# Performance work log

Hardware: AMD Instinct MI355X
Metric: run time of the kernel (lower is better)

## Reference

```python
import jax, jax.numpy as jnp
import numpy as np

N_NODES = 100000
N_EDGES = 1600000
NUM_FEATURES = 128
HIDDEN_DIM = 64
NUM_CLASSES = 2
NUM_GRAPHS = 128


def setup_inputs() -> dict:
    key = jax.random.key(0)
    ks = jax.random.split(key, 9)
    x = jax.random.normal(ks[0], (N_NODES, NUM_FEATURES), dtype=jnp.float32)
    edge_index = jax.random.randint(ks[1], (2, N_EDGES), 0, N_NODES, dtype=jnp.int64)
    batch = jnp.sort(jax.random.randint(ks[2], (N_NODES,), 0, NUM_GRAPHS, dtype=jnp.int64))
    # GCNConv weights (PyG: glorot-init linear, zero bias; values here arbitrary for a numeric baseline)
    s1 = 1.0 / np.sqrt(NUM_FEATURES)
    s2 = 1.0 / np.sqrt(HIDDEN_DIM)
    W1 = jax.random.uniform(ks[3], (NUM_FEATURES, HIDDEN_DIM), jnp.float32, -s1, s1)
    b1 = jax.random.uniform(ks[4], (HIDDEN_DIM,), jnp.float32, -s1, s1)
    W2 = jax.random.uniform(ks[5], (HIDDEN_DIM, HIDDEN_DIM), jnp.float32, -s2, s2)
    b2 = jax.random.uniform(ks[6], (HIDDEN_DIM,), jnp.float32, -s2, s2)
    Wf = jax.random.uniform(ks[7], (HIDDEN_DIM, NUM_CLASSES), jnp.float32, -s2, s2)
    bf = jax.random.uniform(ks[8], (NUM_CLASSES,), jnp.float32, -s2, s2)
    return {"x": x, "edge_index": edge_index, "batch": batch,
            "W1": W1, "b1": b1, "W2": W2, "b2": b2, "Wf": Wf, "bf": bf}


def _gcn_aggregate(h, src, dst, norm, n_nodes):
    # messages: gather source features, scale by sym-norm coefficient, scatter-add at targets
    msg = h[src] * norm[:, None]                       # [E+N, F]
    return jax.ops.segment_sum(msg, dst, num_segments=n_nodes)


def reference(x, edge_index, batch, W1, b1, W2, b2, Wf, bf):
    n = x.shape[0]
    loops = jnp.arange(n, dtype=edge_index.dtype)
    # GCNConv adds self-loops and uses symmetric normalization D^{-1/2}(A+I)D^{-1/2}
    src = jnp.concatenate([edge_index[0], loops])
    dst = jnp.concatenate([edge_index[1], loops])
    deg = jax.ops.segment_sum(jnp.ones_like(dst, dtype=x.dtype), dst, num_segments=n)
    dis = jnp.where(deg > 0, jax.lax.rsqrt(jnp.maximum(deg, 1.0)), 0.0)
    norm = dis[src] * dis[dst]                         # per-edge coefficient

    h = jax.nn.relu(_gcn_aggregate(x @ W1, src, dst, norm, n) + b1)
    h = jax.nn.relu(_gcn_aggregate(h @ W2, src, dst, norm, n) + b2)

    # global_mean_pool over batch segment ids
    sums = jax.ops.segment_sum(h, batch, num_segments=NUM_GRAPHS)
    counts = jax.ops.segment_sum(jnp.ones((n,), dtype=h.dtype), batch, num_segments=NUM_GRAPHS)
    pooled = sums / jnp.maximum(counts, 1.0)[:, None]  # [G, hidden]

    return pooled @ Wf + bf                            # [G, num_classes]
```

## Files before the change

kernel.cpp:

```cpp
#include <hip/hip_runtime.h>
#include <hip/hip_bf16.h>


constexpr int F_IN   = 128;
constexpr int HID    = 64;
constexpr int NGRAPH = 128;
constexpr int NCLS   = 2;

constexpr int EPB = 4096;
constexpr int NB  = 391;
constexpr int DPB = 256;
constexpr int ST  = 56;
constexpr int NOCT = ST / 8;

typedef __attribute__((ext_vector_type(8))) short bf16x8;
typedef __attribute__((ext_vector_type(4))) float f32x4;

__device__ __forceinline__ float bf2f(unsigned short s) {
    union { unsigned u; float f; } v; v.u = ((unsigned)s) << 16; return v.f;
}
__device__ __forceinline__ unsigned short f2bf(float f) {
    union { float f; unsigned u; } v; v.f = f;
    unsigned u = v.u;
    return (unsigned short)((u + 0x7FFFu + ((u >> 16) & 1u)) >> 16);
}
__device__ __forceinline__ void unpack8(uint4 g, float* f) {
    union { unsigned u; float x; } v;
    v.u = g.x << 16; f[0] = v.x;  v.u = g.x & 0xFFFF0000u; f[1] = v.x;
    v.u = g.y << 16; f[2] = v.x;  v.u = g.y & 0xFFFF0000u; f[3] = v.x;
    v.u = g.z << 16; f[4] = v.x;  v.u = g.z & 0xFFFF0000u; f[5] = v.x;
    v.u = g.w << 16; f[6] = v.x;  v.u = g.w & 0xFFFF0000u; f[7] = v.x;
}

__global__ __launch_bounds__(256) void k_bin2(const int* __restrict__ srcv,
                                              const int* __restrict__ dstv,
                                              int* __restrict__ gcur,
                                              unsigned* __restrict__ bin,
                                              int E, int cap) {
    __shared__ int h[NB];
    __shared__ int base[NB];
    for (int i = threadIdx.x; i < NB; i += 256) h[i] = 0;
    __syncthreads();
    int e0 = blockIdx.x * EPB, e1 = min(e0 + EPB, E);
    for (int e = e0 + threadIdx.x; e < e1; e += 256)
        atomicAdd(&h[dstv[e] >> 8], 1);
    __syncthreads();
    for (int i = threadIdx.x; i < NB; i += 256) {
        int c = h[i];
        base[i] = (c > 0) ? atomicAdd(&gcur[i], c) : 0;
        h[i] = 0;
    }
    __syncthreads();
    for (int e = e0 + threadIdx.x; e < e1; e += 256) {
        int d = dstv[e], s = srcv[e];
        int b = d >> 8;
        int pos = base[b] + atomicAdd(&h[b], 1);
        bin[(size_t)b * cap + pos] = ((unsigned)(d & 255) << 20) | (unsigned)s;
    }
}

__global__ __launch_bounds__(256) void k_ell(const unsigned* __restrict__ bin,
                                             const int* __restrict__ bktCnt,
                                             int* __restrict__ ellg,
                                             int* __restrict__ cntg,
                                             float* __restrict__ disg,
                                             int N, int cap) {
    __shared__ int lcnt[DPB];
    __shared__ int lell[DPB * ST];
    int b = blockIdx.x;
    for (int i = threadIdx.x; i < DPB; i += 256) lcnt[i] = 0;
    for (int i = threadIdx.x; i < DPB * ST; i += 256) lell[i] = -1;
    __syncthreads();
    int n = bktCnt[b];
    const unsigned* src = bin + (size_t)b * cap;
    for (int i = threadIdx.x; i < n; i += 256) {
        unsigned p = src[i];
        int d = (int)(p >> 20);
        int s = (int)(p & 0xFFFFF);
        int pos = atomicAdd(&lcnt[d], 1);
        if (pos < ST) lell[d * ST + pos] = s;
    }
    __syncthreads();
    int base = b * DPB;
    int lim = (N - base) * ST;
    if (lim > DPB * ST) lim = DPB * ST;
    int* dst = ellg + (size_t)base * ST;
    for (int i = threadIdx.x; i < lim; i += 256) dst[i] = lell[i];
    for (int i = threadIdx.x; i < DPB; i += 256) {
        int r = base + i;
        if (r < N) {
            int c = min(lcnt[i], ST);
            cntg[r] = c;
            disg[r] = rsqrtf((float)c + 1.0f);
        }
    }
}

__global__ __launch_bounds__(256) void k_gemm_f(const float* __restrict__ X,
                                                const float* __restrict__ W,
                                                unsigned short* __restrict__ Y,
                                                int M) {
    constexpr int SRX = 136;
    constexpr int SRW = 136;
    __shared__ unsigned short Xs[128 * SRX];
    __shared__ unsigned short Wt[64 * SRW];
    const int t = threadIdx.x;
    const int row0 = blockIdx.x * 128;

#pragma unroll
    for (int i = 0; i < 16; ++i) {
        int idx = i * 256 + t;
        int r = idx >> 5, c4 = idx & 31;
        int gr = row0 + r;
        float4 v = (gr < M) ? *(const float4*)&X[(size_t)gr * 128 + c4 * 4]
                            : float4{0.f, 0.f, 0.f, 0.f};
        uint2 p{f2bf(v.x) | ((unsigned)f2bf(v.y) << 16),
                f2bf(v.z) | ((unsigned)f2bf(v.w) << 16)};
        *(uint2*)&Xs[r * SRX + c4 * 4] = p;
    }
#pragma unroll
    for (int i = 0; i < 8; ++i) {
        int idx = i * 256 + t;
        int k = idx >> 4, n4 = idx & 15;
        float4 v = *(const float4*)&W[(size_t)k * 64 + n4 * 4];
        Wt[(n4 * 4 + 0) * SRW + k] = f2bf(v.x);
        Wt[(n4 * 4 + 1) * SRW + k] = f2bf(v.y);
        Wt[(n4 * 4 + 2) * SRW + k] = f2bf(v.z);
        Wt[(n4 * 4 + 3) * SRW + k] = f2bf(v.w);
    }
    __syncthreads();

    const int ln = t & 63, wv = t >> 6;
    const int m16 = ln & 15, kg = ln >> 4;
    const int rbase = wv * 32;
    f32x4 acc[2][4];
#pragma unroll
    for (int i = 0; i < 2; ++i)
#pragma unroll
        for (int j = 0; j < 4; ++j) acc[i][j] = f32x4{0.f, 0.f, 0.f, 0.f};

#pragma unroll
    for (int ks = 0; ks < 4; ++ks) {
        bf16x8 a0 = *(const bf16x8*)&Xs[(rbase + m16) * SRX + ks * 32 + kg * 8];
        bf16x8 a1 = *(const bf16x8*)&Xs[(rbase + 16 + m16) * SRX + ks * 32 + kg * 8];
#pragma unroll
        for (int ct = 0; ct < 4; ++ct) {
            bf16x8 b = *(const bf16x8*)&Wt[(ct * 16 + m16) * SRW + ks * 32 + kg * 8];
            acc[0][ct] = __builtin_amdgcn_mfma_f32_16x16x32_bf16(a0, b, acc[0][ct], 0, 0, 0);
            acc[1][ct] = __builtin_amdgcn_mfma_f32_16x16x32_bf16(a1, b, acc[1][ct], 0, 0, 0);
        }
    }

    __syncthreads();
    unsigned short* Cs = Xs;
#pragma unroll
    for (int mt = 0; mt < 2; ++mt)
#pragma unroll
        for (int ct = 0; ct < 4; ++ct)
#pragma unroll
            for (int reg = 0; reg < 4; ++reg) {
                int r = rbase + mt * 16 + kg * 4 + reg;
                Cs[r * 64 + ct * 16 + m16] = f2bf(acc[mt][ct][reg]);
            }
    __syncthreads();
#pragma unroll
    for (int i = 0; i < 4; ++i) {
        int idx = i * 256 + t;
        int r = idx >> 3, c8 = idx & 7;
        int gr = row0 + r;
        if (gr < M)
            *(uint4*)&Y[(size_t)gr * 64 + c8 * 8] = *(const uint4*)&Cs[r * 64 + c8 * 8];
    }
}

__global__ __launch_bounds__(256) void k_gemm_b(const unsigned short* __restrict__ X,
                                                const float* __restrict__ W,
                                                unsigned short* __restrict__ Y,
                                                int M) {
    constexpr int SRX = 72;
    constexpr int SRW = 72;
    __shared__ unsigned short Xs[128 * SRX];
    __shared__ unsigned short Wt[64 * SRW];
    const int t = threadIdx.x;
    const int row0 = blockIdx.x * 128;

#pragma unroll
    for (int i = 0; i < 4; ++i) {
        int idx = i * 256 + t;
        int r = idx >> 3, c8 = idx & 7;
        int gr = row0 + r;
        uint4 v = (gr < M) ? *(const uint4*)&X[(size_t)gr * 64 + c8 * 8]
                           : uint4{0u, 0u, 0u, 0u};
        *(uint4*)&Xs[r * SRX + c8 * 8] = v;
    }
#pragma unroll
    for (int i = 0; i < 4; ++i) {
        int idx = i * 256 + t;
        int k = idx >> 4, n4 = idx & 15;
        float4 v = *(const float4*)&W[(size_t)k * 64 + n4 * 4];
        Wt[(n4 * 4 + 0) * SRW + k] = f2bf(v.x);
        Wt[(n4 * 4 + 1) * SRW + k] = f2bf(v.y);
        Wt[(n4 * 4 + 2) * SRW + k] = f2bf(v.z);
        Wt[(n4 * 4 + 3) * SRW + k] = f2bf(v.w);
    }
    __syncthreads();

    const int ln = t & 63, wv = t >> 6;
    const int m16 = ln & 15, kg = ln >> 4;
    const int rbase = wv * 32;
    f32x4 acc[2][4];
#pragma unroll
    for (int i = 0; i < 2; ++i)
#pragma unroll
        for (int j = 0; j < 4; ++j) acc[i][j] = f32x4{0.f, 0.f, 0.f, 0.f};

#pragma unroll
    for (int ks = 0; ks < 2; ++ks) {
        bf16x8 a0 = *(const bf16x8*)&Xs[(rbase + m16) * SRX + ks * 32 + kg * 8];
        bf16x8 a1 = *(const bf16x8*)&Xs[(rbase + 16 + m16) * SRX + ks * 32 + kg * 8];
#pragma unroll
        for (int ct = 0; ct < 4; ++ct) {
            bf16x8 b = *(const bf16x8*)&Wt[(ct * 16 + m16) * SRW + ks * 32 + kg * 8];
            acc[0][ct] = __builtin_amdgcn_mfma_f32_16x16x32_bf16(a0, b, acc[0][ct], 0, 0, 0);
            acc[1][ct] = __builtin_amdgcn_mfma_f32_16x16x32_bf16(a1, b, acc[1][ct], 0, 0, 0);
        }
    }

    __syncthreads();
    unsigned short* Cs = Xs;
#pragma unroll
    for (int mt = 0; mt < 2; ++mt)
#pragma unroll
        for (int ct = 0; ct < 4; ++ct)
#pragma unroll
            for (int reg = 0; reg < 4; ++reg) {
                int r = rbase + mt * 16 + kg * 4 + reg;
                Cs[r * 64 + ct * 16 + m16] = f2bf(acc[mt][ct][reg]);
            }
    __syncthreads();
#pragma unroll
    for (int i = 0; i < 4; ++i) {
        int idx = i * 256 + t;
        int r = idx >> 3, c8 = idx & 7;
        int gr = row0 + r;
        if (gr < M)
            *(uint4*)&Y[(size_t)gr * 64 + c8 * 8] = *(const uint4*)&Cs[r * 64 + c8 * 8];
    }
}

__global__ __launch_bounds__(256) void k_gather(const unsigned short* __restrict__ h,
                                                const int* __restrict__ ell,
                                                const int* __restrict__ cnt,
                                                const float* __restrict__ dis,
                                                const float* __restrict__ b,
                                                unsigned short* __restrict__ outb,
                                                int N) {
    int wave = (blockIdx.x * 256 + threadIdx.x) >> 6;
    int lane = threadIdx.x & 63;
    int nq   = lane >> 3;
    int sl   = lane & 7;
    int node = wave * 8 + nq;
    bool valid = node < N;
    int nc = valid ? node : N - 1;

    int deg  = cnt[nc];
    float dd = dis[nc];
    const uint4* h4 = (const uint4*)h;

    int raws[NOCT];
#pragma unroll
    for (int o = 0; o < NOCT; ++o)
        raws[o] = (o * 8 + sl < deg) ? ell[(size_t)nc * ST + o * 8 + sl] : -1;

    int   idxs[NOCT];
    float wsv[NOCT];
#pragma unroll
    for (int o = 0; o < NOCT; ++o) {
        idxs[o] = (raws[o] >= 0) ? raws[o] : 0;
        wsv[o]  = (raws[o] >= 0) ? dis[idxs[o]] * dd : 0.f;
    }

    float acc[8], tmp[8];
    unpack8(h4[(size_t)nc * 8 + sl], acc);
    float sw = dd * dd;
    float4 bv0 = *(const float4*)&b[sl * 8];
    float4 bv1 = *(const float4*)&b[sl * 8 + 4];
    acc[0] = acc[0] * sw + bv0.x; acc[1] = acc[1] * sw + bv0.y;
    acc[2] = acc[2] * sw + bv0.z; acc[3] = acc[3] * sw + bv0.w;
    acc[4] = acc[4] * sw + bv1.x; acc[5] = acc[5] * sw + bv1.y;
    acc[6] = acc[6] * sw + bv1.z; acc[7] = acc[7] * sw + bv1.w;

#pragma unroll
    for (int o = 0; o < NOCT; ++o) {
        if (o * 8 < deg) {
#pragma unroll
            for (int jj = 0; jj < 8; ++jj) {
                int   s  = __shfl(idxs[o], nq * 8 + jj, 64);
                float wj = __shfl(wsv[o],  nq * 8 + jj, 64);
                uint4 g = h4[(size_t)s * 8 + sl];
                unpack8(g, tmp);
#pragma unroll
                for (int q = 0; q < 8; ++q)
                    acc[q] = fmaf(tmp[q], wj, acc[q]);
            }
        }
    }
    if (valid) {
        uint4 p;
        p.x = f2bf(fmaxf(acc[0], 0.f)) | ((unsigned)f2bf(fmaxf(acc[1], 0.f)) << 16);
        p.y = f2bf(fmaxf(acc[2], 0.f)) | ((unsigned)f2bf(fmaxf(acc[3], 0.f)) << 16);
        p.z = f2bf(fmaxf(acc[4], 0.f)) | ((unsigned)f2bf(fmaxf(acc[5], 0.f)) << 16);
        p.w = f2bf(fmaxf(acc[6], 0.f)) | ((unsigned)f2bf(fmaxf(acc[7], 0.f)) << 16);
        ((uint4*)outb)[(size_t)node * 8 + sl] = p;
    }
}

constexpr int POOL_CHUNK = 16;
__global__ __launch_bounds__(256) void k_pool(const unsigned short* __restrict__ h,
                                              const int* __restrict__ batch,
                                              float* __restrict__ sums,
                                              float* __restrict__ gcnt, int N) {
    int wave = (blockIdx.x * 256 + threadIdx.x) >> 6;
    int lane = threadIdx.x & 63;
    int n0 = wave * POOL_CHUNK;
    if (n0 >= N) return;
    int n1 = min(n0 + POOL_CHUNK, N);

    int   gcur = batch[n0];
    float acc  = 0.f;
    int   run  = 0;
    for (int n = n0; n < n1; ++n) {
        int g = batch[n];
        if (g != gcur) {
            atomicAdd(&sums[gcur * HID + lane], acc);
            if (lane == 0) atomicAdd(&gcnt[gcur], (float)run);
            gcur = g; acc = 0.f; run = 0;
        }
        acc += bf2f(h[(size_t)n * HID + lane]);
        ++run;
    }
    atomicAdd(&sums[gcur * HID + lane], acc);
    if (lane == 0) atomicAdd(&gcnt[gcur], (float)run);
}

__global__ __launch_bounds__(256) void k_final(const float* __restrict__ sums,
                                               const float* __restrict__ gcnt,
                                               const float* __restrict__ Wf,
                                               const float* __restrict__ bfv,
                                               float* __restrict__ out) {
    int t = threadIdx.x;
    int g = t >> 1, c = t & 1;
    float invc = 1.0f / fmaxf(gcnt[g], 1.0f);
    float acc = bfv[c];
#pragma unroll
    for (int k = 0; k < HID; ++k)
        acc = fmaf(sums[g * HID + k] * invc, Wf[k * NCLS + c], acc);
    out[g * NCLS + c] = acc;
}

extern "C" void kernel_launch(void* const* d_in, const int* in_sizes, int n_in,
                              void* d_out, int out_size, void* d_ws, size_t ws_size,
                              hipStream_t stream) {
    const float* x   = (const float*)d_in[0];
    const int*   ei  = (const int*)d_in[1];
    const int*   bat = (const int*)d_in[2];
    const float* W1  = (const float*)d_in[3];
    const float* b1  = (const float*)d_in[4];
    const float* W2  = (const float*)d_in[5];
    const float* b2  = (const float*)d_in[6];
    const float* Wf  = (const float*)d_in[7];
    const float* bfv = (const float*)d_in[8];
    float* out = (float*)d_out;

    const int N = in_sizes[0] / F_IN;
    const int E = in_sizes[1] / 2;
    const int* srcv = ei;
    const int* dstv = ei + E;

    const int nblk = (E + EPB - 1) / EPB;
    const int cap  = E / NB + 1280;

    const size_t S2 = (size_t)N * HID * 2;
    char* ws = (char*)d_ws;
    unsigned short* bufA = (unsigned short*)ws;
    unsigned short* bufB = (unsigned short*)(ws + S2);
    int*   ell  = (int*)(ws + 2 * S2);
    char*  tail = ws + 2 * S2 + (size_t)N * ST * 4;
    int*   cnt  = (int*)tail;
    float* dis  = (float*)(tail + (size_t)N * 4);
    float* sums = (float*)(tail + (size_t)N * 8);
    float* gcnt = sums + NGRAPH * HID;
    int*   gcur = (int*)(gcnt + NGRAPH);

    unsigned* bin = (unsigned*)bufA;

    hipMemsetAsync(sums, 0, (size_t)(NGRAPH * HID + NGRAPH + NB) * 4, stream);

    k_bin2<<<nblk, 256, 0, stream>>>(srcv, dstv, gcur, bin, E, cap);
    k_ell<<<NB, 256, 0, stream>>>(bin, gcur, ell, cnt, dis, N, cap);

    const int gemmBlk = (N + 127) / 128;
    const int gathBlk = (N + 31) / 32;
    k_gemm_f<<<gemmBlk, 256, 0, stream>>>(x, W1, bufA, N);
    k_gather<<<gathBlk, 256, 0, stream>>>(bufA, ell, cnt, dis, b1, bufB, N);

    k_gemm_b<<<gemmBlk, 256, 0, stream>>>(bufB, W2, bufA, N);
    k_gather<<<gathBlk, 256, 0, stream>>>(bufA, ell, cnt, dis, b2, bufB, N);

    const int poolBlk = (((N + POOL_CHUNK - 1) / POOL_CHUNK) + 3) / 4;
    k_pool<<<poolBlk, 256, 0, stream>>>(bufB, bat, sums, gcnt, N);
    k_final<<<1, 256, 0, stream>>>(sums, gcnt, Wf, bfv, out);
}
```

Measured before the change: 267.2 us.

## Process two nodes per lane-group in gather and stage edges in LDS for binning

The gather kernel now has each 8-lane group handle two nodes, interleaving their neighbor loads to raise memory-level parallelism. It drops the per-node degree check and always walks all ST slots, relying on -1 padding and zero weights. That adds wasted loads of row 0 for low-degree nodes. The binning kernel caches dst/src in shared memory so the second pass no longer re-reads global memory, at the cost of 32KB of LDS per block.

```diff
diff --git a/kernel.cpp b/kernel.cpp
--- a/kernel.cpp
+++ b/kernel.cpp
@@ -39,11 +39,16 @@
                                               int E, int cap) {
     __shared__ int h[NB];
     __shared__ int base[NB];
+    __shared__ int ld[EPB];
+    __shared__ int ls[EPB];
     for (int i = threadIdx.x; i < NB; i += 256) h[i] = 0;
     __syncthreads();
-    int e0 = blockIdx.x * EPB, e1 = min(e0 + EPB, E);
-    for (int e = e0 + threadIdx.x; e < e1; e += 256)
-        atomicAdd(&h[dstv[e] >> 8], 1);
+    int e0 = blockIdx.x * EPB, e1 = min(e0 + EPB, E), n = e1 - e0;
+    for (int i = threadIdx.x; i < n; i += 256) {
+        int d = dstv[e0 + i], s = srcv[e0 + i];
+        ld[i] = d; ls[i] = s;
+        atomicAdd(&h[d >> 8], 1);
+    }
     __syncthreads();
     for (int i = threadIdx.x; i < NB; i += 256) {
         int c = h[i];
@@ -51,8 +56,8 @@
         h[i] = 0;
     }
     __syncthreads();
-    for (int e = e0 + threadIdx.x; e < e1; e += 256) {
-        int d = dstv[e], s = srcv[e];
+    for (int i = threadIdx.x; i < n; i += 256) {
+        int d = ld[i], s = ls[i];
         int b = d >> 8;
         int pos = base[b] + atomicAdd(&h[b], 1);
         bin[(size_t)b * cap + pos] = ((unsigned)(d & 255) << 20) | (unsigned)s;
@@ -250,7 +255,6 @@
 
 __global__ __launch_bounds__(256) void k_gather(const unsigned short* __restrict__ h,
                                                 const int* __restrict__ ell,
-                                                const int* __restrict__ cnt,
                                                 const float* __restrict__ dis,
                                                 const float* __restrict__ b,
                                                 unsigned short* __restrict__ outb,
@@ -259,59 +263,87 @@
     int lane = threadIdx.x & 63;
     int nq   = lane >> 3;
     int sl   = lane & 7;
-    int node = wave * 8 + nq;
-    bool valid = node < N;
-    int nc = valid ? node : N - 1;
-
-    int deg  = cnt[nc];
-    float dd = dis[nc];
+    int nodeA = wave * 16 + nq;
+    int nodeB = wave * 16 + 8 + nq;
+    bool vA = nodeA < N, vB = nodeB < N;
+    int ncA = vA ? nodeA : N - 1;
+    int ncB = vB ? nodeB : N - 1;
+
+    float ddA = dis[ncA], ddB = dis[ncB];
     const uint4* h4 = (const uint4*)h;
-
-    int raws[NOCT];
-#pragma unroll
-    for (int o = 0; o < NOCT; ++o)
-        raws[o] = (o * 8 + sl < deg) ? ell[(size_t)nc * ST + o * 8 + sl] : -1;
-
-    int   idxs[NOCT];
-    float wsv[NOCT];
+    const int* ellA = ell + (size_t)ncA * ST;
+    const int* ellB = ell + (size_t)ncB * ST;
+
+    int rawA[NOCT], rawB[NOCT];
 #pragma unroll
     for (int o = 0; o < NOCT; ++o) {
-        idxs[o] = (raws[o] >= 0) ? raws[o] : 0;
-        wsv[o]  = (raws[o] >= 0) ? dis[idxs[o]] * dd : 0.f;
-    }
-
-    float acc[8], tmp[8];
-    unpack8(h4[(size_t)nc * 8 + sl], acc);
-    float sw = dd * dd;
-    float4 bv0 = *(const float4*)&b[sl * 8];
-    float4 bv1 = *(const float4*)&b[sl * 8 + 4];
-    acc[0] = acc[0] * sw + bv0.x; acc[1] = acc[1] * sw + bv0.y;
-    acc[2] = acc[2] * sw + bv0.z; acc[3] = acc[3] * sw + bv0.w;
-    acc[4] = acc[4] * sw + bv1.x; acc[5] = acc[5] * sw + bv1.y;
-    acc[6] = acc[6] * sw + bv1.z; acc[7] = acc[7] * sw + bv1.w;
-
+        rawA[o] = ellA[o * 8 + sl];
+        rawB[o] = ellB[o * 8 + sl];
+    }
+    int   idxA[NOCT], idxB[NOCT];
+    float wA[NOCT],  wB[NOCT];
 #pragma unroll
     for (int o = 0; o < NOCT; ++o) {
-        if (o * 8 < deg) {
-#pragma unroll
-            for (int jj = 0; jj < 8; ++jj) {
-                int   s  = __shfl(idxs[o], nq * 8 + jj, 64);
-                float wj = __shfl(wsv[o],  nq * 8 + jj, 64);
-                uint4 g = h4[(size_t)s * 8 + sl];
-                unpack8(g, tmp);
-#pragma unroll
-                for (int q = 0; q < 8; ++q)
-                    acc[q] = fmaf(tmp[q], wj, acc[q]);
+        idxA[o] = (rawA[o] >= 0) ? rawA[o] : 0;
+        wA[o]   = (rawA[o] >= 0) ? dis[idxA[o]] * ddA : 0.f;
+        idxB[o] = (rawB[o] >= 0) ? rawB[o] : 0;
+        wB[o]   = (rawB[o] >= 0) ? dis[idxB[o]] * ddB : 0.f;
+    }
+
+    float accA[8], accB[8];
+    {
+        float4 bv0 = *(const float4*)&b[sl * 8];
+        float4 bv1 = *(const float4*)&b[sl * 8 + 4];
+        float tA[8], tB[8];
+        unpack8(h4[(size_t)ncA * 8 + sl], tA);
+        unpack8(h4[(size_t)ncB * 8 + sl], tB);
+        float swA = ddA * ddA, swB = ddB * ddB;
+        accA[0] = tA[0] * swA + bv0.x; accA[1] = tA[1] * swA + bv0.y;
+        accA[2] = tA[2] * swA + bv0.z; accA[3] = tA[3] * swA + bv0.w;
+        accA[4] = tA[4] * swA + bv1.x; accA[5] = tA[5] * swA + bv1.y;
+        accA[6] = tA[6] * swA + bv1.z; accA[7] = tA[7] * swA + bv1.w;
+        accB[0] = tB[0] * swB + bv0.x; accB[1] = tB[1] * swB + bv0.y;
+        accB[2] = tB[2] * swB + bv0.z; accB[3] = tB[3] * swB + bv0.w;
+        accB[4] = tB[4] * swB + bv1.x; accB[5] = tB[5] * swB + bv1.y;
+        accB[6] = tB[6] * swB + bv1.z; accB[7] = tB[7] * swB + bv1.w;
+    }
+
+#pragma unroll
+    for (int o = 0; o < NOCT; ++o) {
+#pragma unroll
+        for (int jj = 0; jj < 8; ++jj) {
+            int   sA = __shfl(idxA[o], nq * 8 + jj, 64);
+            float fA = __shfl(wA[o],   nq * 8 + jj, 64);
+            int   sB = __shfl(idxB[o], nq * 8 + jj, 64);
+            float fB = __shfl(wB[o],   nq * 8 + jj, 64);
+            uint4 gA = h4[(size_t)sA * 8 + sl];
+            uint4 gB = h4[(size_t)sB * 8 + sl];
+            float tA[8], tB[8];
+            unpack8(gA, tA);
+            unpack8(gB, tB);
+#pragma unroll
+            for (int q = 0; q < 8; ++q) {
+                accA[q] = fmaf(tA[q], fA, accA[q]);
+                accB[q] = fmaf(tB[q], fB, accB[q]);
             }
         }
     }
-    if (valid) {
+
+    if (vA) {
         uint4 p;
-        p.x = f2bf(fmaxf(acc[0], 0.f)) | ((unsigned)f2bf(fmaxf(acc[1], 0.f)) << 16);
-        p.y = f2bf(fmaxf(acc[2], 0.f)) | ((unsigned)f2bf(fmaxf(acc[3], 0.f)) << 16);
-        p.z = f2bf(fmaxf(acc[4], 0.f)) | ((unsigned)f2bf(fmaxf(acc[5], 0.f)) << 16);
-        p.w = f2bf(fmaxf(acc[6], 0.f)) | ((unsigned)f2bf(fmaxf(acc[7], 0.f)) << 16);
-        ((uint4*)outb)[(size_t)node * 8 + sl] = p;
+        p.x = f2bf(fmaxf(accA[0], 0.f)) | ((unsigned)f2bf(fmaxf(accA[1], 0.f)) << 16);
+        p.y = f2bf(fmaxf(accA[2], 0.f)) | ((unsigned)f2bf(fmaxf(accA[3], 0.f)) << 16);
+        p.z = f2bf(fmaxf(accA[4], 0.f)) | ((unsigned)f2bf(fmaxf(accA[5], 0.f)) << 16);
+        p.w = f2bf(fmaxf(accA[6], 0.f)) | ((unsigned)f2bf(fmaxf(accA[7], 0.f)) << 16);
+        ((uint4*)outb)[(size_t)nodeA * 8 + sl] = p;
+    }
+    if (vB) {
+        uint4 p;
+        p.x = f2bf(fmaxf(accB[0], 0.f)) | ((unsigned)f2bf(fmaxf(accB[1], 0.f)) << 16);
+        p.y = f2bf(fmaxf(accB[2], 0.f)) | ((unsigned)f2bf(fmaxf(accB[3], 0.f)) << 16);
+        p.z = f2bf(fmaxf(accB[4], 0.f)) | ((unsigned)f2bf(fmaxf(accB[5], 0.f)) << 16);
+        p.w = f2bf(fmaxf(accB[6], 0.f)) | ((unsigned)f2bf(fmaxf(accB[7], 0.f)) << 16);
+        ((uint4*)outb)[(size_t)nodeB * 8 + sl] = p;
     }
 }
 
@@ -400,12 +432,12 @@
     k_ell<<<NB, 256, 0, stream>>>(bin, gcur, ell, cnt, dis, N, cap);
 
     const int gemmBlk = (N + 127) / 128;
-    const int gathBlk = (N + 31) / 32;
+    const int gathBlk = (N + 63) / 64;
     k_gemm_f<<<gemmBlk, 256, 0, stream>>>(x, W1, bufA, N);
-    k_gather<<<gathBlk, 256, 0, stream>>>(bufA, ell, cnt, dis, b1, bufB, N);
+    k_gather<<<gathBlk, 256, 0, stream>>>(bufA, ell, dis, b1, bufB, N);
 
     k_gemm_b<<<gemmBlk, 256, 0, stream>>>(bufB, W2, bufA, N);
-    k_gather<<<gathBlk, 256, 0, stream>>>(bufA, ell, cnt, dis, b2, bufB, N);
+    k_gather<<<gathBlk, 256, 0, stream>>>(bufA, ell, dis, b2, bufB, N);
 
     const int poolBlk = (((N + POOL_CHUNK - 1) / POOL_CHUNK) + 3) / 4;
     k_pool<<<poolBlk, 256, 0, stream>>>(bufB, bat, sums, gcnt, N);
```

After: 769.7 us. 2.88x slower.
